# Kernel optimization log

Hardware: AMD Instinct MI355X
Metric: run time of the kernel (lower is better)

## Reference

```python
import jax, jax.numpy as jnp
import numpy as np
from jax import lax

B, C, H, W = 4, 64, 64, 64
CH = C // 2  # edge_detect hidden channels
BN_EPS = 1e-5


def conv1x1(x, w, b):
    # x: (B,C,H,W), w: (O,C), b: (O,)
    return jnp.einsum('bchw,oc->bohw', x, w) + b[None, :, None, None]


def setup_inputs() -> dict:
    key = jax.random.key(0)
    ks = jax.random.split(key, 12)
    s = 1.0 / np.sqrt(C)
    inp = {
        'x': jax.random.normal(ks[0], (B, C, H, W), jnp.float32),
        'Wq': jax.random.normal(ks[1], (C, C), jnp.float32) * s,
        'bq': jnp.zeros((C,), jnp.float32),
        'Wk': jax.random.normal(ks[2], (C, C), jnp.float32) * s,
        'bk': jnp.zeros((C,), jnp.float32),
        'Wv': jax.random.normal(ks[3], (C, C), jnp.float32) * s,
        'bv': jnp.zeros((C,), jnp.float32),
        'We1': jax.random.normal(ks[4], (CH, C, 3, 3), jnp.float32) * (1.0 / np.sqrt(C * 9)),
        'be1': jnp.zeros((CH,), jnp.float32),
        'bn_w': jnp.ones((CH,), jnp.float32),
        'bn_b': jnp.zeros((CH,), jnp.float32),
        'bn_mean': jnp.zeros((CH,), jnp.float32),
        'bn_var': jnp.ones((CH,), jnp.float32),
        'We2': jax.random.normal(ks[5], (1, CH), jnp.float32) * (1.0 / np.sqrt(CH)),
        'be2': jnp.zeros((1,), jnp.float32),
        'gamma': jax.random.normal(ks[6], (1,), jnp.float32) * 0.1,
        'beta': jax.random.normal(ks[7], (1,), jnp.float32) * 0.1,
    }
    return inp


def reference(x, Wq, bq, Wk, bk, Wv, bv, We1, be1, bn_w, bn_b, bn_mean, bn_var, We2, be2, gamma, beta):
    b, c, h, w = x.shape
    hw = h * w
    q = conv1x1(x, Wq, bq).reshape(b, c, hw).transpose(0, 2, 1)  # (B,HW,C)
    k = conv1x1(x, Wk, bk).reshape(b, c, hw)                      # (B,C,HW)
    v = conv1x1(x, Wv, bv).reshape(b, c, hw)                      # (B,C,HW)

    energy = jnp.einsum('bnc,bcm->bnm', q, k)                      # (B,HW,HW)
    attention = jax.nn.softmax(energy, axis=-1)

    # edge_detect: 3x3 conv -> BN (eval stats) -> ReLU -> 1x1 conv -> sigmoid
    e = lax.conv_general_dilated(x, We1, (1, 1), 'SAME',
                                 dimension_numbers=('NCHW', 'OIHW', 'NCHW'))
    e = e + be1[None, :, None, None]
    e = (e - bn_mean[None, :, None, None]) * jax.lax.rsqrt(bn_var + BN_EPS)[None, :, None, None]
    e = e * bn_w[None, :, None, None] + bn_b[None, :, None, None]
    e = jax.nn.relu(e)
    e = conv1x1(e, We2, be2)                                       # (B,1,H,W)
    edge = jax.nn.sigmoid(e).reshape(b, 1, hw)                     # (B,1,HW)

    fa = attention * (1.0 + beta[0] * edge)                        # broadcast over query dim
    denom = jnp.maximum(jnp.sum(jnp.abs(fa), axis=2, keepdims=True), 1e-12)
    fa = fa / denom                                                # L1 renorm along keys

    out = jnp.einsum('bcm,bnm->bcn', v, fa).reshape(b, c, h, w)
    return gamma[0] * out + x
```

## Files before the change

### kernel.cpp

```cpp
#include <hip/hip_runtime.h>
#include <hip/hip_bf16.h>

typedef unsigned short u16;
typedef __attribute__((ext_vector_type(8))) __bf16 bf16x8;
typedef __attribute__((ext_vector_type(4))) float f32x4;


__device__ __forceinline__ u16 f2bf(float f) {
    unsigned u = __builtin_bit_cast(unsigned, f);
    u += 0x7FFFu + ((u >> 16) & 1u);
    return (u16)(u >> 16);
}
__device__ __forceinline__ float bf2f(u16 v) {
    unsigned u = ((unsigned)v) << 16;
    return __builtin_bit_cast(float, u);
}

__global__ __launch_bounds__(256) void qkv_edge_kernel(
    const float* __restrict__ x,
    const float* __restrict__ Wq, const float* __restrict__ bq,
    const float* __restrict__ Wk, const float* __restrict__ bk,
    const float* __restrict__ Wv, const float* __restrict__ bv,
    const float* __restrict__ We1, const float* __restrict__ be1,
    const float* __restrict__ bn_w, const float* __restrict__ bn_b,
    const float* __restrict__ bn_mean, const float* __restrict__ bn_var,
    const float* __restrict__ We2, const float* __restrict__ be2,
    const float* __restrict__ beta,
    u16* __restrict__ Qt, u16* __restrict__ Kt, u16* __restrict__ Vm,
    float* __restrict__ wkey)
{
    __shared__ __align__(16) u16 sm[33280];
    const int t = threadIdx.x;
    const int wv = t >> 6, lane = t & 63;
    const int quad = lane >> 4, l15 = lane & 15;

    if (blockIdx.x < 256) {
        u16* Wl   = sm;
        u16* xt_s = sm + 13824;
        u16* vt   = sm + 13824 + 4224;
        const int b = blockIdx.x >> 6;
        const int n0 = (blockIdx.x & 63) << 6;

        const float* Wmat[3] = {Wq, Wk, Wv};
#pragma unroll
        for (int m = 0; m < 3; ++m)
#pragma unroll
            for (int i = 0; i < 4; ++i) {
                int u = t + i * 256;
                float4 w4 = *reinterpret_cast<const float4*>(Wmat[m] + u * 4);
                int row = u >> 4, col = (u & 15) * 4;
                uint2 pk;
                pk.x = (unsigned)f2bf(w4.x) | ((unsigned)f2bf(w4.y) << 16);
                pk.y = (unsigned)f2bf(w4.z) | ((unsigned)f2bf(w4.w) << 16);
                *reinterpret_cast<uint2*>(&Wl[(m * 64 + row) * 72 + col]) = pk;
            }
        for (int i = 0; i < 16; ++i) {
            int lin = t + i * 256;
            int c = lin >> 6, nn = lin & 63;
            xt_s[nn * 66 + c] = f2bf(x[(size_t)(b * 64 + c) * 4096 + n0 + nn]);
        }
        __syncthreads();

        bf16x8 bx[2];
#pragma unroll
        for (int h = 0; h < 2; ++h)
            bx[h] = *reinterpret_cast<const bf16x8*>(
                &xt_s[(wv * 16 + l15) * 66 + h * 32 + quad * 8]);

        f32x4 d[3][4];
#pragma unroll
        for (int m = 0; m < 3; ++m)
#pragma unroll
            for (int mt = 0; mt < 4; ++mt) d[m][mt] = (f32x4){0.f, 0.f, 0.f, 0.f};

#pragma unroll
        for (int h = 0; h < 2; ++h)
#pragma unroll
            for (int m = 0; m < 3; ++m)
#pragma unroll
                for (int mt = 0; mt < 4; ++mt) {
                    bf16x8 af = *reinterpret_cast<const bf16x8*>(
                        &Wl[(m * 64 + mt * 16 + l15) * 72 + h * 32 + quad * 8]);
                    d[m][mt] = __builtin_amdgcn_mfma_f32_16x16x32_bf16(af, bx[h], d[m][mt], 0, 0, 0);
                }

        const float* bias[3] = {bq, bk, bv};
        const float L2E = 1.44269504f;
#pragma unroll
        for (int m = 0; m < 3; ++m)
#pragma unroll
            for (int mt = 0; mt < 4; ++mt) {
                float4 bi = *reinterpret_cast<const float4*>(bias[m] + mt * 16 + quad * 4);
                d[m][mt][0] += bi.x; d[m][mt][1] += bi.y; d[m][mt][2] += bi.z; d[m][mt][3] += bi.w;
                if (m == 0) {
                    d[m][mt][0] *= L2E; d[m][mt][1] *= L2E;
                    d[m][mt][2] *= L2E; d[m][mt][3] *= L2E;
                }
            }

        const int rowchunk = (n0 >> 4) + wv;
#pragma unroll
        for (int m = 0; m < 2; ++m) {
            u16* base = (m == 0 ? Qt : Kt) + (size_t)b * 262144;
#pragma unroll
            for (int mt = 0; mt < 4; ++mt) {
                uint2 pk;
                pk.x = (unsigned)f2bf(d[m][mt][0]) | ((unsigned)f2bf(d[m][mt][1]) << 16);
                pk.y = (unsigned)f2bf(d[m][mt][2]) | ((unsigned)f2bf(d[m][mt][3]) << 16);
                *reinterpret_cast<uint2*>(
                    base + ((size_t)(rowchunk * 8 + mt * 2 + (quad >> 1))) * 128 +
                    l15 * 8 + (quad & 1) * 4) = pk;
            }
        }
#pragma unroll
        for (int mt = 0; mt < 4; ++mt)
#pragma unroll
            for (int r = 0; r < 4; ++r)
                vt[(mt * 16 + quad * 4 + r) * 72 + wv * 16 + l15] = f2bf(d[2][mt][r]);
        __syncthreads();
        {
            u16* Vb_st = Vm + (size_t)b * 262144;
            const int kt = n0 >> 6;
#pragma unroll
            for (int i = 0; i < 2; ++i) {
                int unit = t + i * 256;
                int f = unit >> 7, hq = (unit >> 4) & 7, cl = unit & 15;
                const u16* src = &vt[(f * 16 + cl) * 72 + hq * 8];
                uint4 v4 = *reinterpret_cast<const uint4*>(src);
                *reinterpret_cast<uint4*>(
                    Vb_st + ((size_t)((kt * 4 + f) * 8 + hq)) * 128 + cl * 8) = v4;
            }
        }
    } else {
        u16* Ae_s = sm;
        u16* xr_s = sm + 18688;
        const int eb = blockIdx.x - 256;
        const int b = eb >> 6, h = eb & 63;

        if (t < 192) {
            int kh = t / 64, rem = t & 63;
            int col = (rem >> 5) * 65, ci2 = (rem & 31) * 2;
            *reinterpret_cast<unsigned*>(&xr_s[(kh * 66 + col) * 72 + ci2]) = 0u;
        }
#pragma unroll
        for (int i = 0; i < 18; ++i) {
            int u = t + i * 256;
            int ch = u / 144;
            int rem = u - ch * 144;
            int p = rem >> 4, cig = (rem & 15) * 4;
            const float* src = We1 + ch * 576 + cig * 9 + p;
            float a = src[0], b2 = src[9], c2 = src[18], d2 = src[27];
            uint2 pk;
            pk.x = (unsigned)f2bf(a) | ((unsigned)f2bf(b2) << 16);
            pk.y = (unsigned)f2bf(c2) | ((unsigned)f2bf(d2) << 16);
            *reinterpret_cast<uint2*>(&Ae_s[ch * 584 + p * 64 + cig]) = pk;
        }
#pragma unroll
        for (int i = 0; i < 12; ++i) {
            int u = t + i * 256;
            int w = u & 63, cig = (u >> 6) & 15, kh = u >> 10;
            int hs = h + kh - 1;
            float v0 = 0.f, v1 = 0.f, v2 = 0.f, v3 = 0.f;
            if ((unsigned)hs < 64u) {
                const float* src = x + ((size_t)(b * 64 + cig * 4) * 64 + hs) * 64 + w;
                v0 = src[0]; v1 = src[4096]; v2 = src[8192]; v3 = src[12288];
            }
            uint2 pk;
            pk.x = (unsigned)f2bf(v0) | ((unsigned)f2bf(v1) << 16);
            pk.y = (unsigned)f2bf(v2) | ((unsigned)f2bf(v3) << 16);
            *reinterpret_cast<uint2*>(&xr_s[(kh * 66 + w + 1) * 72 + cig * 4]) = pk;
        }
        __syncthreads();

        f32x4 e[2];
        e[0] = (f32x4){0.f, 0.f, 0.f, 0.f};
        e[1] = (f32x4){0.f, 0.f, 0.f, 0.f};
#pragma unroll
        for (int p = 0; p < 9; ++p) {
            const int kh = p / 3, kw = p - kh * 3;
#pragma unroll
            for (int half = 0; half < 2; ++half) {
                bf16x8 bfr = *reinterpret_cast<const bf16x8*>(
                    &xr_s[(kh * 66 + wv * 16 + l15 + kw) * 72 + half * 32 + quad * 8]);
#pragma unroll
                for (int mt = 0; mt < 2; ++mt) {
                    bf16x8 af = *reinterpret_cast<const bf16x8*>(
                        &Ae_s[(mt * 16 + l15) * 584 + p * 64 + half * 32 + quad * 8]);
                    e[mt] = __builtin_amdgcn_mfma_f32_16x16x32_bf16(af, bfr, e[mt], 0, 0, 0);
                }
            }
        }
        float partial = 0.f;
#pragma unroll
        for (int mt = 0; mt < 2; ++mt) {
            float4 bw = *reinterpret_cast<const float4*>(bn_w    + mt * 16 + quad * 4);
            float4 bb = *reinterpret_cast<const float4*>(bn_b    + mt * 16 + quad * 4);
            float4 bm = *reinterpret_cast<const float4*>(bn_mean + mt * 16 + quad * 4);
            float4 bv2 = *reinterpret_cast<const float4*>(bn_var + mt * 16 + quad * 4);
            float4 b1 = *reinterpret_cast<const float4*>(be1     + mt * 16 + quad * 4);
            float4 w2 = *reinterpret_cast<const float4*>(We2     + mt * 16 + quad * 4);
            float sc, sh;
            sc = bw.x * rsqrtf(bv2.x + 1e-5f); sh = (b1.x - bm.x) * sc + bb.x;
            partial += fmaxf(e[mt][0] * sc + sh, 0.f) * w2.x;
            sc = bw.y * rsqrtf(bv2.y + 1e-5f); sh = (b1.y - bm.y) * sc + bb.y;
            partial += fmaxf(e[mt][1] * sc + sh, 0.f) * w2.y;
            sc = bw.z * rsqrtf(bv2.z + 1e-5f); sh = (b1.z - bm.z) * sc + bb.z;
            partial += fmaxf(e[mt][2] * sc + sh, 0.f) * w2.z;
            sc = bw.w * rsqrtf(bv2.w + 1e-5f); sh = (b1.w - bm.w) * sc + bb.w;
            partial += fmaxf(e[mt][3] * sc + sh, 0.f) * w2.w;
        }
        partial += __shfl_xor(partial, 16);
        partial += __shfl_xor(partial, 32);
        if (lane < 16) {
            float s = partial + be2[0];
            float sg = 1.f / (1.f + __expf(-s));
            wkey[(size_t)b * 4096 + h * 64 + wv * 16 + lane] = 1.f + beta[0] * sg;
        }
    }
}

template <int NSPLIT>
__global__ __launch_bounds__(128, 2) void attn_kernel(
    const u16* __restrict__ Qt, const u16* __restrict__ Kt,
    const u16* __restrict__ Vm, const float* __restrict__ wkey,
    u16* __restrict__ O_part, float* __restrict__ l_part)
{
    constexpr int KT_ITERS = 64 / NSPLIT;
    const int t = threadIdx.x;
    const int qi = blockIdx.x / NSPLIT;
    const int split = blockIdx.x % NSPLIT;
    const int b = qi >> 6;
    const int n0 = (qi & 63) << 6;
    const int wv = t >> 6, lane = t & 63;
    const int quad = lane >> 4, l15 = lane & 15;

    const int src0 = ((quad & 1) * 2) * 16 + l15;
    const int src1 = src0 + 16;
    const bool msel = (quad >> 1) != 0;

    const u16* Qb = Qt + (size_t)b * 262144;
    const u16* Kb = Kt + (size_t)b * 262144;
    const u16* Vb = Vm + (size_t)b * 262144;
    const float* wb = wkey + (size_t)b * 4096;

    bf16x8 qf[2][2];
#pragma unroll
    for (int nt = 0; nt < 2; ++nt)
#pragma unroll
        for (int h = 0; h < 2; ++h)
            qf[nt][h] = __builtin_bit_cast(bf16x8, *reinterpret_cast<const uint4*>(
                Qb + ((size_t)(((n0 >> 4) + wv * 2 + nt) * 8 + h * 4 + quad)) * 128 + l15 * 8));

    const int kt0 = split * KT_ITERS;
    uint4 kf[4][2];
    float4 wf[4];
#pragma unroll
    for (int mt = 0; mt < 4; ++mt) {
#pragma unroll
        for (int h = 0; h < 2; ++h)
            kf[mt][h] = *reinterpret_cast<const uint4*>(
                Kb + ((size_t)((kt0 * 4 + mt) * 8 + h * 4 + quad)) * 128 + l15 * 8);
        wf[mt] = *reinterpret_cast<const float4*>(wb + kt0 * 64 + mt * 16 + quad * 4);
    }

    const uint4 ones_u = {0x3F803F80u, 0x3F803F80u, 0x3F803F80u, 0x3F803F80u};
    const bf16x8 onesf = __builtin_bit_cast(bf16x8, ones_u);

    f32x4 o[4][2];
    f32x4 l5[2];
#pragma unroll
    for (int fc = 0; fc < 4; ++fc)
#pragma unroll
        for (int nt = 0; nt < 2; ++nt) o[fc][nt] = (f32x4){0.f, 0.f, 0.f, 0.f};
#pragma unroll
    for (int nt = 0; nt < 2; ++nt) l5[nt] = (f32x4){0.f, 0.f, 0.f, 0.f};

    for (int kt = kt0; kt < kt0 + KT_ITERS; ++kt) {
        uint4 vf[4][2];
#pragma unroll
        for (int f = 0; f < 4; ++f)
#pragma unroll
            for (int h = 0; h < 2; ++h)
                vf[f][h] = *reinterpret_cast<const uint4*>(
                    Vb + ((size_t)((kt * 4 + f) * 8 + h * 4 + quad)) * 128 + l15 * 8);

        f32x4 s[4][2];
#pragma unroll
        for (int mt = 0; mt < 4; ++mt)
#pragma unroll
            for (int nt = 0; nt < 2; ++nt) {
                f32x4 a = (f32x4){0.f, 0.f, 0.f, 0.f};
                a = __builtin_amdgcn_mfma_f32_16x16x32_bf16(
                        __builtin_bit_cast(bf16x8, kf[mt][0]), qf[nt][0], a, 0, 0, 0);
                a = __builtin_amdgcn_mfma_f32_16x16x32_bf16(
                        __builtin_bit_cast(bf16x8, kf[mt][1]), qf[nt][1], a, 0, 0, 0);
                s[mt][nt] = a;
            }

        const int ktn = (kt + 1 < kt0 + KT_ITERS) ? kt + 1 : kt0;
#pragma unroll
        for (int mt = 0; mt < 4; ++mt)
#pragma unroll
            for (int h = 0; h < 2; ++h)
                kf[mt][h] = *reinterpret_cast<const uint4*>(
                    Kb + ((size_t)((ktn * 4 + mt) * 8 + h * 4 + quad)) * 128 + l15 * 8);

        uint2 pk[4][2];
        const float OFF = 17.3123405f;
#pragma unroll
        for (int mt = 0; mt < 4; ++mt) {
            const float* wfp = reinterpret_cast<const float*>(&wf[mt]);
#pragma unroll
            for (int nt = 0; nt < 2; ++nt) {
                float p0 = exp2f(s[mt][nt][0] - OFF) * wfp[0];
                float p1 = exp2f(s[mt][nt][1] - OFF) * wfp[1];
                float p2 = exp2f(s[mt][nt][2] - OFF) * wfp[2];
                float p3 = exp2f(s[mt][nt][3] - OFF) * wfp[3];
                unsigned u0 = __builtin_bit_cast(unsigned, p0);
                unsigned u1 = __builtin_bit_cast(unsigned, p1);
                unsigned u2 = __builtin_bit_cast(unsigned, p2);
                unsigned u3 = __builtin_bit_cast(unsigned, p3);
                pk[mt][nt].x = (u0 >> 16) | (u1 & 0xFFFF0000u);
                pk[mt][nt].y = (u2 >> 16) | (u3 & 0xFFFF0000u);
            }
        }

#pragma unroll
        for (int mt = 0; mt < 4; ++mt)
            wf[mt] = *reinterpret_cast<const float4*>(wb + ktn * 64 + mt * 16 + quad * 4);

        bf16x8 pb[2][2];
#pragma unroll
        for (int h = 0; h < 2; ++h)
#pragma unroll
            for (int nt = 0; nt < 2; ++nt) {
                unsigned a0x = (unsigned)__shfl((int)pk[h * 2][nt].x, src0, 64);
                unsigned a1x = (unsigned)__shfl((int)pk[h * 2 + 1][nt].x, src0, 64);
                unsigned a0y = (unsigned)__shfl((int)pk[h * 2][nt].y, src0, 64);
                unsigned a1y = (unsigned)__shfl((int)pk[h * 2 + 1][nt].y, src0, 64);
                unsigned a0z = (unsigned)__shfl((int)pk[h * 2][nt].x, src1, 64);
                unsigned a1z = (unsigned)__shfl((int)pk[h * 2 + 1][nt].x, src1, 64);
                unsigned a0w = (unsigned)__shfl((int)pk[h * 2][nt].y, src1, 64);
                unsigned a1w = (unsigned)__shfl((int)pk[h * 2 + 1][nt].y, src1, 64);
                uint4 g;
                g.x = msel ? a1x : a0x;
                g.y = msel ? a1y : a0y;
                g.z = msel ? a1z : a0z;
                g.w = msel ? a1w : a0w;
                pb[nt][h] = __builtin_bit_cast(bf16x8, g);
            }

#pragma unroll
        for (int nt = 0; nt < 2; ++nt) {
#pragma unroll
            for (int fc = 0; fc < 4; ++fc) {
                o[fc][nt] = __builtin_amdgcn_mfma_f32_16x16x32_bf16(
                    __builtin_bit_cast(bf16x8, vf[fc][0]), pb[nt][0], o[fc][nt], 0, 0, 0);
                o[fc][nt] = __builtin_amdgcn_mfma_f32_16x16x32_bf16(
                    __builtin_bit_cast(bf16x8, vf[fc][1]), pb[nt][1], o[fc][nt], 0, 0, 0);
            }
            l5[nt] = __builtin_amdgcn_mfma_f32_16x16x32_bf16(onesf, pb[nt][0], l5[nt], 0, 0, 0);
            l5[nt] = __builtin_amdgcn_mfma_f32_16x16x32_bf16(onesf, pb[nt][1], l5[nt], 0, 0, 0);
        }
    }

    const size_t pbase = (size_t)blockIdx.x * 4096;
#pragma unroll
    for (int nt = 0; nt < 2; ++nt) {
        if (quad == 0)
            l_part[(size_t)blockIdx.x * 64 + wv * 32 + nt * 16 + l15] = l5[nt][0];
#pragma unroll
        for (int fc = 0; fc < 4; ++fc) {
            uint2 pk2;
            pk2.x = (unsigned)f2bf(o[fc][nt][0]) | ((unsigned)f2bf(o[fc][nt][1]) << 16);
            pk2.y = (unsigned)f2bf(o[fc][nt][2]) | ((unsigned)f2bf(o[fc][nt][3]) << 16);
            *reinterpret_cast<uint2*>(
                &O_part[pbase + ((((wv * 2 + nt) * 4 + fc) * 4 + quad)) * 64 + l15 * 4]) = pk2;
        }
    }
}

template <int NSPLIT>
__global__ __launch_bounds__(256) void combine_kernel(
    const u16* __restrict__ O_part, const float* __restrict__ l_part,
    const float* __restrict__ x, const float* __restrict__ g_gamma,
    float* __restrict__ out)
{
    __shared__ float ot[64 * 68];
    __shared__ float ls[64];
    const int t = threadIdx.x;
    const int qi = blockIdx.x;
    const int b = qi >> 6;
    const int n0 = (qi & 63) << 6;
    const int f = t >> 6, quad = (t >> 4) & 3, l15 = t & 15;
    const float gamma = g_gamma[0];

    float acc[2][2][4];
#pragma unroll
    for (int wv = 0; wv < 2; ++wv)
#pragma unroll
        for (int nt = 0; nt < 2; ++nt)
#pragma unroll
            for (int r = 0; r < 4; ++r) acc[wv][nt][r] = 0.f;

#pragma unroll
    for (int s4 = 0; s4 < NSPLIT; ++s4) {
        const u16* base = O_part + ((size_t)(qi * NSPLIT + s4)) * 4096;
#pragma unroll
        for (int wv = 0; wv < 2; ++wv)
#pragma unroll
            for (int nt = 0; nt < 2; ++nt) {
                uint2 u = *reinterpret_cast<const uint2*>(
                    base + ((((wv * 2 + nt) * 4 + f) * 4 + quad)) * 64 + l15 * 4);
                acc[wv][nt][0] += bf2f((u16)(u.x & 0xFFFF));
                acc[wv][nt][1] += bf2f((u16)(u.x >> 16));
                acc[wv][nt][2] += bf2f((u16)(u.y & 0xFFFF));
                acc[wv][nt][3] += bf2f((u16)(u.y >> 16));
            }
    }
#pragma unroll
    for (int wv = 0; wv < 2; ++wv)
#pragma unroll
        for (int nt = 0; nt < 2; ++nt) {
            float4 v4;
            v4.x = acc[wv][nt][0]; v4.y = acc[wv][nt][1];
            v4.z = acc[wv][nt][2]; v4.w = acc[wv][nt][3];
            *reinterpret_cast<float4*>(
                &ot[(wv * 32 + nt * 16 + l15) * 68 + f * 16 + quad * 4]) = v4;
        }
    if (t < 64) {
        float lsum = 0.f;
#pragma unroll
        for (int s4 = 0; s4 < NSPLIT; ++s4)
            lsum += l_part[((size_t)(qi * NSPLIT + s4)) * 64 + t];
        ls[t] = gamma / fmaxf(lsum, 1e-30f);
    }
    __syncthreads();
    {
        const int c = t >> 2, nseg = t & 3;
        const size_t gbase = ((size_t)(b * 64 + c)) * 4096 + n0 + nseg * 16;
#pragma unroll
        for (int j = 0; j < 4; ++j) {
            float4 xv = *reinterpret_cast<const float4*>(&x[gbase + j * 4]);
            float4 rv;
            int nl = nseg * 16 + j * 4;
            rv.x = ot[(nl + 0) * 68 + c] * ls[nl + 0] + xv.x;
            rv.y = ot[(nl + 1) * 68 + c] * ls[nl + 1] + xv.y;
            rv.z = ot[(nl + 2) * 68 + c] * ls[nl + 2] + xv.z;
            rv.w = ot[(nl + 3) * 68 + c] * ls[nl + 3] + xv.w;
            *reinterpret_cast<float4*>(&out[gbase + j * 4]) = rv;
        }
    }
}

extern "C" void kernel_launch(void* const* d_in, const int* in_sizes, int n_in,
                              void* d_out, int out_size, void* d_ws, size_t ws_size,
                              hipStream_t stream) {
    const float* x      = (const float*)d_in[0];
    const float* Wq     = (const float*)d_in[1];
    const float* bq     = (const float*)d_in[2];
    const float* Wk     = (const float*)d_in[3];
    const float* bk     = (const float*)d_in[4];
    const float* Wv     = (const float*)d_in[5];
    const float* bv     = (const float*)d_in[6];
    const float* We1    = (const float*)d_in[7];
    const float* be1    = (const float*)d_in[8];
    const float* bn_w   = (const float*)d_in[9];
    const float* bn_b   = (const float*)d_in[10];
    const float* bn_mean= (const float*)d_in[11];
    const float* bn_var = (const float*)d_in[12];
    const float* We2    = (const float*)d_in[13];
    const float* be2    = (const float*)d_in[14];
    const float* gamma  = (const float*)d_in[15];
    const float* beta   = (const float*)d_in[16];

    char* ws = (char*)d_ws;
    const size_t KB = 1024, MB = 1024 * 1024;
    u16*   Qt     = (u16*)ws;
    u16*   Kt     = (u16*)(ws + 2 * MB);
    u16*   Vm     = (u16*)(ws + 4 * MB);
    float* wkey   = (float*)(ws + 6 * MB);
    float* l_part = (float*)(ws + 6 * MB + 64 * KB);
    u16*   O_part = (u16*)(ws + 6 * MB + 576 * KB);

    const bool use8 = ws_size >= (6 * MB + 576 * KB + (size_t)2048 * 64 * 64 * 2);

    float* out = (float*)d_out;

    qkv_edge_kernel<<<dim3(512), dim3(256), 0, stream>>>(
        x, Wq, bq, Wk, bk, Wv, bv, We1, be1, bn_w, bn_b, bn_mean, bn_var,
        We2, be2, beta, Qt, Kt, Vm, wkey);
    if (use8) {
        attn_kernel<8><<<dim3(2048), dim3(128), 0, stream>>>(Qt, Kt, Vm, wkey, O_part, l_part);
        combine_kernel<8><<<dim3(256), dim3(256), 0, stream>>>(O_part, l_part, x, gamma, out);
    } else {
        attn_kernel<4><<<dim3(1024), dim3(128), 0, stream>>>(Qt, Kt, Vm, wkey, O_part, l_part);
        combine_kernel<4><<<dim3(256), dim3(256), 0, stream>>>(O_part, l_part, x, gamma, out);
    }
}
```

Measured before the change: 140.1 us.

## Fix split count at four and split combine kernel into quarter-row blocks

Removes the workspace-dependent choice between 8 and 4 key splits and always uses 4, halving partial-output traffic and combine reduction work. The combine kernel is restructured so each block handles 16 query rows instead of 64, launching four times as many smaller blocks with less shared memory. The trade-off is fewer attention blocks, so less parallelism in the main attention pass.

```diff
diff --git a/kernel.cpp b/kernel.cpp
--- a/kernel.cpp
+++ b/kernel.cpp
@@ -5,6 +5,8 @@
 typedef __attribute__((ext_vector_type(8))) __bf16 bf16x8;
 typedef __attribute__((ext_vector_type(4))) float f32x4;
 
+
+#define NSPLIT 4
 
 __device__ __forceinline__ u16 f2bf(float f) {
     unsigned u = __builtin_bit_cast(unsigned, f);
@@ -219,7 +221,6 @@
     }
 }
 
-template <int NSPLIT>
 __global__ __launch_bounds__(128, 2) void attn_kernel(
     const u16* __restrict__ Qt, const u16* __restrict__ Kt,
     const u16* __restrict__ Vm, const float* __restrict__ wkey,
@@ -380,76 +381,56 @@
     }
 }
 
-template <int NSPLIT>
 __global__ __launch_bounds__(256) void combine_kernel(
     const u16* __restrict__ O_part, const float* __restrict__ l_part,
     const float* __restrict__ x, const float* __restrict__ g_gamma,
     float* __restrict__ out)
 {
-    __shared__ float ot[64 * 68];
-    __shared__ float ls[64];
+    __shared__ float ot[16 * 68];
+    __shared__ float ls[16];
     const int t = threadIdx.x;
-    const int qi = blockIdx.x;
+    const int qi = blockIdx.x >> 2;
+    const int quarter = blockIdx.x & 3;
     const int b = qi >> 6;
     const int n0 = (qi & 63) << 6;
+    const int rbase = (quarter >> 1) * 32 + (quarter & 1) * 16;
     const int f = t >> 6, quad = (t >> 4) & 3, l15 = t & 15;
     const float gamma = g_gamma[0];
 
-    float acc[2][2][4];
-#pragma unroll
-    for (int wv = 0; wv < 2; ++wv)
-#pragma unroll
-        for (int nt = 0; nt < 2; ++nt)
-#pragma unroll
-            for (int r = 0; r < 4; ++r) acc[wv][nt][r] = 0.f;
-
-#pragma unroll
-    for (int s4 = 0; s4 < NSPLIT; ++s4) {
-        const u16* base = O_part + ((size_t)(qi * NSPLIT + s4)) * 4096;
-#pragma unroll
-        for (int wv = 0; wv < 2; ++wv)
-#pragma unroll
-            for (int nt = 0; nt < 2; ++nt) {
-                uint2 u = *reinterpret_cast<const uint2*>(
-                    base + ((((wv * 2 + nt) * 4 + f) * 4 + quad)) * 64 + l15 * 4);
-                acc[wv][nt][0] += bf2f((u16)(u.x & 0xFFFF));
-                acc[wv][nt][1] += bf2f((u16)(u.x >> 16));
-                acc[wv][nt][2] += bf2f((u16)(u.y & 0xFFFF));
-                acc[wv][nt][3] += bf2f((u16)(u.y >> 16));
-            }
-    }
-#pragma unroll
-    for (int wv = 0; wv < 2; ++wv)
-#pragma unroll
-        for (int nt = 0; nt < 2; ++nt) {
-            float4 v4;
-            v4.x = acc[wv][nt][0]; v4.y = acc[wv][nt][1];
-            v4.z = acc[wv][nt][2]; v4.w = acc[wv][nt][3];
-            *reinterpret_cast<float4*>(
-                &ot[(wv * 32 + nt * 16 + l15) * 68 + f * 16 + quad * 4]) = v4;
-        }
-    if (t < 64) {
-        float lsum = 0.f;
-#pragma unroll
-        for (int s4 = 0; s4 < NSPLIT; ++s4)
-            lsum += l_part[((size_t)(qi * NSPLIT + s4)) * 64 + t];
-        ls[t] = gamma / fmaxf(lsum, 1e-30f);
+    {
+        float a0 = 0.f, a1 = 0.f, a2 = 0.f, a3 = 0.f;
+#pragma unroll
+        for (int s4 = 0; s4 < NSPLIT; ++s4) {
+            const u16* base = O_part + ((size_t)(qi * NSPLIT + s4)) * 4096;
+            uint2 u = *reinterpret_cast<const uint2*>(
+                base + (((quarter * 4 + f) * 4 + quad)) * 64 + l15 * 4);
+            a0 += bf2f((u16)(u.x & 0xFFFF));
+            a1 += bf2f((u16)(u.x >> 16));
+            a2 += bf2f((u16)(u.y & 0xFFFF));
+            a3 += bf2f((u16)(u.y >> 16));
+        }
+        float4 v4; v4.x = a0; v4.y = a1; v4.z = a2; v4.w = a3;
+        *reinterpret_cast<float4*>(&ot[l15 * 68 + f * 16 + quad * 4]) = v4;
+        if (t < 16) {
+            float lsum = 0.f;
+#pragma unroll
+            for (int s4 = 0; s4 < NSPLIT; ++s4)
+                lsum += l_part[((size_t)(qi * NSPLIT + s4)) * 64 + rbase + t];
+            ls[t] = gamma / fmaxf(lsum, 1e-30f);
+        }
     }
     __syncthreads();
     {
         const int c = t >> 2, nseg = t & 3;
-        const size_t gbase = ((size_t)(b * 64 + c)) * 4096 + n0 + nseg * 16;
-#pragma unroll
-        for (int j = 0; j < 4; ++j) {
-            float4 xv = *reinterpret_cast<const float4*>(&x[gbase + j * 4]);
-            float4 rv;
-            int nl = nseg * 16 + j * 4;
-            rv.x = ot[(nl + 0) * 68 + c] * ls[nl + 0] + xv.x;
-            rv.y = ot[(nl + 1) * 68 + c] * ls[nl + 1] + xv.y;
-            rv.z = ot[(nl + 2) * 68 + c] * ls[nl + 2] + xv.z;
-            rv.w = ot[(nl + 3) * 68 + c] * ls[nl + 3] + xv.w;
-            *reinterpret_cast<float4*>(&out[gbase + j * 4]) = rv;
-        }
+        const size_t gbase = ((size_t)(b * 64 + c)) * 4096 + n0 + rbase + nseg * 4;
+        float4 xv = *reinterpret_cast<const float4*>(&x[gbase]);
+        float4 rv;
+        int nl = nseg * 4;
+        rv.x = ot[(nl + 0) * 68 + c] * ls[nl + 0] + xv.x;
+        rv.y = ot[(nl + 1) * 68 + c] * ls[nl + 1] + xv.y;
+        rv.z = ot[(nl + 2) * 68 + c] * ls[nl + 2] + xv.z;
+        rv.w = ot[(nl + 3) * 68 + c] * ls[nl + 3] + xv.w;
+        *reinterpret_cast<float4*>(&out[gbase]) = rv;
     }
 }
 
@@ -483,18 +464,13 @@
     float* l_part = (float*)(ws + 6 * MB + 64 * KB);
     u16*   O_part = (u16*)(ws + 6 * MB + 576 * KB);
 
-    const bool use8 = ws_size >= (6 * MB + 576 * KB + (size_t)2048 * 64 * 64 * 2);
-
     float* out = (float*)d_out;
 
     qkv_edge_kernel<<<dim3(512), dim3(256), 0, stream>>>(
         x, Wq, bq, Wk, bk, Wv, bv, We1, be1, bn_w, bn_b, bn_mean, bn_var,
         We2, be2, beta, Qt, Kt, Vm, wkey);
-    if (use8) {
-        attn_kernel<8><<<dim3(2048), dim3(128), 0, stream>>>(Qt, Kt, Vm, wkey, O_part, l_part);
-        combine_kernel<8><<<dim3(256), dim3(256), 0, stream>>>(O_part, l_part, x, gamma, out);
-    } else {
-        attn_kernel<4><<<dim3(1024), dim3(128), 0, stream>>>(Qt, Kt, Vm, wkey, O_part, l_part);
-        combine_kernel<4><<<dim3(256), dim3(256), 0, stream>>>(O_part, l_part, x, gamma, out);
-    }
-}
+    attn_kernel<<<dim3(256 * NSPLIT), dim3(128), 0, stream>>>(
+        Qt, Kt, Vm, wkey, O_part, l_part);
+    combine_kernel<<<dim3(1024), dim3(256), 0, stream>>>(
+        O_part, l_part, x, gamma, out);
+}
```

New measurement: 138.3 us. Within noise of the previous version (-1.3%).
